# Optimization experiments

Measured on AMD Instinct MI355X. Metric: run time of the kernel, lower is better.

Reference implementation:

```python
import jax, jax.numpy as jnp
import numpy as np

F8_MAX = 448.0  # float8_e4m3fn max
F4_MAX = 6.0    # fp4 e2m1 max
BLOCK = 16      # NVFP4 scaling block size along K

# representable |values| of fp4 e2m1 and midpoints for nearest rounding
_LEVELS = jnp.array([0.0, 0.5, 1.0, 1.5, 2.0, 3.0, 4.0, 6.0], dtype=jnp.float32)
_MIDS = (_LEVELS[:-1] + _LEVELS[1:]) * 0.5


def _e2m1_round(a):
    # round-to-nearest fp4 e2m1 value, sign-magnitude
    s = jnp.sign(a)
    m = jnp.clip(jnp.abs(a), 0.0, F4_MAX)
    idx = jnp.searchsorted(_MIDS, m, side='left')
    return s * jnp.take(_LEVELS, idx)


def _e4m3(x):
    # quantize to float8 e4m3 and dequantize back to fp32
    return jnp.clip(x, -F8_MAX, F8_MAX).astype(jnp.float8_e4m3fn).astype(jnp.float32)


def nvfp4_fake_quant(x, s2):
    # x: [..., K]; s2: scalar global scale = 448*6/global_amax
    shp = x.shape
    K = shp[-1]
    xb = x.reshape(shp[:-1] + (K // BLOCK, BLOCK))  # [..., K/16, 16]
    amax = jnp.max(jnp.abs(xb), axis=-1, keepdims=True)
    sf = _e4m3(amax * s2 / F4_MAX)          # stored per-block fp8 scale (cutlass_vec)
    scale = sf / s2                          # per-block dequant scale in real units
    safe = jnp.where(scale > 0.0, scale, 1.0)
    q = _e2m1_round(xb / safe)               # fp4 codes (as values)
    deq = jnp.where(scale > 0.0, q * scale, 0.0)
    return deq.reshape(shp)


def setup_inputs() -> dict:
    key = jax.random.key(0)
    kx, kw, kb, ks = jax.random.split(key, 4)
    K, N = 4096, 4096
    x = jax.random.normal(kx, (4, 2048, K), dtype=jnp.float32)
    weight = jax.random.uniform(kw, (N, K), dtype=jnp.float32)
    bias = jax.random.uniform(kb, (N,), dtype=jnp.float32)
    # fp4_global_scale of a rand(1, K) tensor, as done in the module __init__
    dummy = jax.random.uniform(ks, (1, K), dtype=jnp.float32)
    s_in2 = ((F8_MAX * F4_MAX) / jnp.max(jnp.abs(dummy))).reshape(1)
    return {'x': x, 'weight': weight, 'bias': bias, 's_in2': s_in2}


def reference(x, weight, bias, s_in2):
    s2_in = s_in2.reshape(())
    s2_w = (F8_MAX * F4_MAX) / jnp.max(jnp.abs(weight))  # fp4_global_scale(weight)
    x_dq = nvfp4_fake_quant(x, s2_in)        # fake-quant activations
    w_dq = nvfp4_fake_quant(weight, s2_w)    # dequantized fp4 weight (stored at init)
    # F.linear: [b,s,k] @ [n,k]^T + bias
    return jnp.einsum('bsk,nk->bsn', x_dq, w_dq) + bias
```

## Files before the change

### kernel.cpp

```cpp
#include <hip/hip_runtime.h>
#include <hip/hip_bf16.h>

typedef __attribute__((ext_vector_type(8))) short short8;
typedef __attribute__((ext_vector_type(8))) unsigned short ushort8;
typedef __attribute__((ext_vector_type(4))) float f32x4;
typedef unsigned short ushort;

#define K_DIM 4096
#define N_DIM 4096
#define BK 32
#define NT (K_DIM / BK)


__device__ __forceinline__ float e4m3_rne(float v) {
    if (v >= 0.015625f) {
        unsigned u = __float_as_uint(v);
        unsigned lsb = (u >> 20) & 1u;
        u = (u + 0x7FFFFu + lsb) & 0xFFF00000u;
        return __uint_as_float(u);
    }
    return rintf(v * 512.0f) * 0.001953125f;
}

__device__ __forceinline__ float e2m1_level(float m) {
    float lv = 0.0f;
    lv = (m > 0.25f) ? 0.5f : lv;
    lv = (m > 0.75f) ? 1.0f : lv;
    lv = (m > 1.25f) ? 1.5f : lv;
    lv = (m > 1.75f) ? 2.0f : lv;
    lv = (m > 2.5f)  ? 3.0f : lv;
    lv = (m > 3.5f)  ? 4.0f : lv;
    lv = (m > 5.0f)  ? 6.0f : lv;
    return lv;
}

__device__ __forceinline__ ushort f32_to_bf16_bits(float f) {
    unsigned u = __float_as_uint(f);
    return (ushort)((u + 0x7FFFu + ((u >> 16) & 1u)) >> 16);
}


__global__ void init_kernel(unsigned* amax_bits) { *amax_bits = 0u; }

__global__ void wamax_kernel(const float* __restrict__ w, unsigned* amax_bits, int n4) {
    float m = 0.f;
    const f32x4* w4 = (const f32x4*)w;
    for (int i = blockIdx.x * blockDim.x + threadIdx.x; i < n4; i += gridDim.x * blockDim.x) {
        f32x4 v = w4[i];
        m = fmaxf(m, fmaxf(fmaxf(fabsf(v.x), fabsf(v.y)), fmaxf(fabsf(v.z), fabsf(v.w))));
    }
#pragma unroll
    for (int off = 32; off >= 1; off >>= 1)
        m = fmaxf(m, __shfl_down(m, off));
    __shared__ float red[4];
    const int lane = threadIdx.x & 63, wv = threadIdx.x >> 6;
    if (lane == 0) red[wv] = m;
    __syncthreads();
    if (threadIdx.x == 0) {
        m = fmaxf(fmaxf(red[0], red[1]), fmaxf(red[2], red[3]));
        atomicMax(amax_bits, __float_as_uint(m));
    }
}

__global__ void quant16_kernel(const float* __restrict__ src,
                               const float* __restrict__ s2_ptr,
                               const unsigned* __restrict__ amax_bits,
                               ushort* __restrict__ dst, int nblk) {
    int t = blockIdx.x * blockDim.x + threadIdx.x;
    if (t >= nblk) return;
    float s2;
    if (s2_ptr) s2 = *s2_ptr;
    else        s2 = 2688.0f / __uint_as_float(*amax_bits);

    const f32x4* s = (const f32x4*)src + (size_t)t * 4;
    float vals[16];
    f32x4 v0 = s[0], v1 = s[1], v2 = s[2], v3 = s[3];
#pragma unroll
    for (int i = 0; i < 4; ++i) {
        vals[i] = v0[i]; vals[4 + i] = v1[i]; vals[8 + i] = v2[i]; vals[12 + i] = v3[i];
    }
    float amax = 0.f;
#pragma unroll
    for (int i = 0; i < 16; ++i) amax = fmaxf(amax, fabsf(vals[i]));

    float sf = e4m3_rne(fminf(amax * s2 / 6.0f, 448.0f));
    float scale = sf / s2;

    ushort8 o0, o1;
    if (scale > 0.f) {
#pragma unroll
        for (int i = 0; i < 16; ++i) {
            float r = vals[i] / scale;
            float m = fminf(fabsf(r), 6.0f);
            float q = copysignf(e2m1_level(m), r);
            ushort b = f32_to_bf16_bits(q * scale);
            if (i < 8) o0[i] = b; else o1[i - 8] = b;
        }
    } else {
#pragma unroll
        for (int i = 0; i < 8; ++i) { o0[i] = 0; o1[i] = 0; }
    }
    ushort8* d8 = (ushort8*)(dst + (size_t)t * 16);
    d8[0] = o0;
    d8[1] = o1;
}


__device__ __forceinline__ void gload16(const ushort* g, ushort* l) {
    __builtin_amdgcn_global_load_lds(
        (const __attribute__((address_space(1))) void*)g,
        (__attribute__((address_space(3))) void*)l, 16, 0, 0);
}

#define SYNC(N)                                              \
    asm volatile("s_waitcnt vmcnt(" #N ")" ::: "memory");    \
    __builtin_amdgcn_sched_barrier(0);                       \
    __builtin_amdgcn_s_barrier();                            \
    __builtin_amdgcn_sched_barrier(0)

__global__ __launch_bounds__(512, 2) void gemm8(
    const ushort* __restrict__ Aq, const ushort* __restrict__ Bq,
    const float* __restrict__ bias, float* __restrict__ C,
    int nby, int nchunk) {
    __shared__ ushort lds[4 * 16384];

    const int tid  = threadIdx.x;
    const int lane = tid & 63;
    const int wave = tid >> 6;
    const int wr = wave >> 2;
    const int wc = wave & 3;

    const int swz = (blockIdx.x & 7) * nchunk + (blockIdx.x >> 3);
    const int by = swz % nby, bx = swz / nby;
    const int bm = by * 256, bn = bx * 256;

    const int r0  = tid >> 2;
    const int cg0 = ((tid & 3) - ((r0 >> 1) & 3)) & 3;
    const ushort* sA0 = Aq + (size_t)(bm + r0) * K_DIM + cg0 * 8;
    const ushort* sB0 = Bq + (size_t)(bn + r0) * K_DIM + cg0 * 8;
    ushort* dA0 = &lds[wave * 512];
    ushort* dB0 = &lds[8192 + wave * 512];

    const int pr   = ((lane >> 4) + ((lane & 15) >> 1)) & 3;
    const int idxA = (wr * 128 + (lane & 15)) * 32 + pr * 8;
    const int idxB = 8192 + (wc * 64 + (lane & 15)) * 32 + pr * 8;

    f32x4 acc[8][4];
#pragma unroll
    for (int m = 0; m < 8; ++m)
#pragma unroll
        for (int n = 0; n < 4; ++n) acc[m][n] = (f32x4)(0.f);

#define STAGE(t) {                                                         \
        const size_t ko = (size_t)(t) * BK;                                \
        const int bb = ((t) & 3) * 16384;                                  \
        gload16(sA0 + ko,                          dA0 + bb);              \
        gload16(sA0 + (size_t)128 * K_DIM + ko,    dA0 + bb + 4096);       \
        gload16(sB0 + ko,                          dB0 + bb);              \
        gload16(sB0 + (size_t)128 * K_DIM + ko,    dB0 + bb + 4096); }

    auto compute = [&](int bufo) {
        const ushort* Lb = &lds[bufo];
        short8 af[8], bfr[4];
#pragma unroll
        for (int m = 0; m < 8; ++m) af[m]  = *(const short8*)(Lb + idxA + m * 512);
#pragma unroll
        for (int n = 0; n < 4; ++n) bfr[n] = *(const short8*)(Lb + idxB + n * 512);
#pragma unroll
        for (int m = 0; m < 8; ++m)
#pragma unroll
            for (int n = 0; n < 4; ++n)
                acc[m][n] = __builtin_amdgcn_mfma_f32_16x16x32_bf16(af[m], bfr[n], acc[m][n], 0, 0, 0);
    };

    STAGE(0); STAGE(1); STAGE(2);
    SYNC(8);

    for (int t = 0; t < NT - 3; ++t) {
        STAGE(t + 3);
        compute((t & 3) * 16384);
        SYNC(8);
    }
    compute(((NT - 3) & 3) * 16384);
    SYNC(4);
    compute(((NT - 2) & 3) * 16384);
    SYNC(0);
    compute(((NT - 1) & 3) * 16384);

    const int fq = lane >> 4, fr = lane & 15;
    float bv[4];
#pragma unroll
    for (int n = 0; n < 4; ++n) bv[n] = bias[bn + wc * 64 + n * 16 + fr];
#pragma unroll
    for (int m = 0; m < 8; ++m)
#pragma unroll
        for (int r = 0; r < 4; ++r) {
            const int row = bm + wr * 128 + m * 16 + fq * 4 + r;
            float* Cr = C + (size_t)row * N_DIM + bn + wc * 64 + fr;
#pragma unroll
            for (int n = 0; n < 4; ++n) Cr[n * 16] = acc[m][n][r] + bv[n];
        }
#undef STAGE
}


extern "C" void kernel_launch(void* const* d_in, const int* in_sizes, int n_in,
                              void* d_out, int out_size, void* d_ws, size_t ws_size,
                              hipStream_t stream) {
    const float* x     = (const float*)d_in[0];
    const float* w     = (const float*)d_in[1];
    const float* bias  = (const float*)d_in[2];
    const float* s_in2 = (const float*)d_in[3];
    float* out = (float*)d_out;

    const int M = in_sizes[0] / K_DIM;

    unsigned* amax_bits = (unsigned*)d_ws;
    ushort* xq = (ushort*)((char*)d_ws + 256);
    ushort* wq = (ushort*)((char*)d_ws + 256 + (size_t)M * K_DIM * 2);

    init_kernel<<<1, 1, 0, stream>>>(amax_bits);
    wamax_kernel<<<1024, 256, 0, stream>>>(w, amax_bits, (N_DIM * K_DIM) / 4);

    const int nblk_x = (M * K_DIM) / 16;
    quant16_kernel<<<nblk_x / 256, 256, 0, stream>>>(x, s_in2, nullptr, xq, nblk_x);
    const int nblk_w = (N_DIM * K_DIM) / 16;
    quant16_kernel<<<nblk_w / 256, 256, 0, stream>>>(w, nullptr, amax_bits, wq, nblk_w);

    const int nby = M / 256;
    const int nwg = nby * (N_DIM / 256);
    gemm8<<<nwg, 512, 0, stream>>>(xq, wq, bias, out, nby, nwg / 8);
}
```

Before: 320.7 us.

## Split GEMM main loop into two barrier-separated phases with interleaved loads and priority

Restructures the GEMM K-loop so each tile is processed in two halves: the first half loads A/B fragments from LDS, issues the A global-to-LDS prefetch, then runs MFMAs at raised wave priority, and the second half does the same with the B prefetch. The aim is to spread global loads and LDS reads across the MFMA work and keep waves in lockstep with extra barriers, ping-pong style. It also replaces the single-thread init kernel with hipMemsetAsync. The extra barriers per iteration add synchronisation cost and may not help if the schedule was already overlapping well.

```diff
diff --git a/kernel.cpp b/kernel.cpp
--- a/kernel.cpp
+++ b/kernel.cpp
@@ -40,8 +40,6 @@
 }
 
 
-__global__ void init_kernel(unsigned* amax_bits) { *amax_bits = 0u; }
-
 __global__ void wamax_kernel(const float* __restrict__ w, unsigned* amax_bits, int n4) {
     float m = 0.f;
     const f32x4* w4 = (const f32x4*)w;
@@ -112,11 +110,7 @@
         (__attribute__((address_space(3))) void*)l, 16, 0, 0);
 }
 
-#define SYNC(N)                                              \
-    asm volatile("s_waitcnt vmcnt(" #N ")" ::: "memory");    \
-    __builtin_amdgcn_sched_barrier(0);                       \
-    __builtin_amdgcn_s_barrier();                            \
-    __builtin_amdgcn_sched_barrier(0)
+#define NOPSTMT ((void)0)
 
 __global__ __launch_bounds__(512, 2) void gemm8(
     const ushort* __restrict__ Aq, const ushort* __restrict__ Bq,
@@ -151,41 +145,90 @@
 #pragma unroll
         for (int n = 0; n < 4; ++n) acc[m][n] = (f32x4)(0.f);
 
-#define STAGE(t) {                                                         \
-        const size_t ko = (size_t)(t) * BK;                                \
-        const int bb = ((t) & 3) * 16384;                                  \
-        gload16(sA0 + ko,                          dA0 + bb);              \
-        gload16(sA0 + (size_t)128 * K_DIM + ko,    dA0 + bb + 4096);       \
-        gload16(sB0 + ko,                          dB0 + bb);              \
-        gload16(sB0 + (size_t)128 * K_DIM + ko,    dB0 + bb + 4096); }
-
-    auto compute = [&](int bufo) {
-        const ushort* Lb = &lds[bufo];
-        short8 af[8], bfr[4];
-#pragma unroll
-        for (int m = 0; m < 8; ++m) af[m]  = *(const short8*)(Lb + idxA + m * 512);
-#pragma unroll
-        for (int n = 0; n < 4; ++n) bfr[n] = *(const short8*)(Lb + idxB + n * 512);
-#pragma unroll
-        for (int m = 0; m < 8; ++m)
-#pragma unroll
-            for (int n = 0; n < 4; ++n)
-                acc[m][n] = __builtin_amdgcn_mfma_f32_16x16x32_bf16(af[m], bfr[n], acc[m][n], 0, 0, 0);
-    };
-
-    STAGE(0); STAGE(1); STAGE(2);
-    SYNC(8);
+    short8 af[8], bfr[4];
+
+#define STAGE_A(t) { const size_t ko = (size_t)(t) * BK;                    \
+        const int bb = ((t) & 3) * 16384;                                   \
+        gload16(sA0 + ko,                       dA0 + bb);                  \
+        gload16(sA0 + (size_t)128 * K_DIM + ko, dA0 + bb + 4096); }
+#define STAGE_B(t) { const size_t ko = (size_t)(t) * BK;                    \
+        const int bb = ((t) & 3) * 16384;                                   \
+        gload16(sB0 + ko,                       dB0 + bb);                  \
+        gload16(sB0 + (size_t)128 * K_DIM + ko, dB0 + bb + 4096); }
+
+#define PHASE0(STAGE_STMT, bufo)                                            \
+    {                                                                       \
+        const ushort* Lb = &lds[bufo];                                      \
+        _Pragma("unroll")                                                   \
+        for (int m = 0; m < 4; ++m) af[m]  = *(const short8*)(Lb + idxA + m * 512); \
+        _Pragma("unroll")                                                   \
+        for (int n = 0; n < 4; ++n) bfr[n] = *(const short8*)(Lb + idxB + n * 512); \
+        STAGE_STMT;                                                         \
+        __builtin_amdgcn_sched_barrier(0);                                  \
+        __builtin_amdgcn_s_barrier();                                       \
+        asm volatile("s_waitcnt lgkmcnt(0)" ::: "memory");                  \
+        __builtin_amdgcn_sched_barrier(0);                                  \
+        __builtin_amdgcn_s_setprio(1);                                      \
+        _Pragma("unroll")                                                   \
+        for (int m = 0; m < 4; ++m)                                         \
+            _Pragma("unroll")                                               \
+            for (int n = 0; n < 4; ++n)                                     \
+                acc[m][n] = __builtin_amdgcn_mfma_f32_16x16x32_bf16(af[m], bfr[n], acc[m][n], 0, 0, 0); \
+        __builtin_amdgcn_s_setprio(0);                                      \
+        __builtin_amdgcn_sched_barrier(0);                                  \
+        __builtin_amdgcn_s_barrier();                                       \
+    }
+
+#define PHASE1(STAGE_STMT, bufo, VN)                                        \
+    {                                                                       \
+        const ushort* Lb = &lds[bufo];                                      \
+        _Pragma("unroll")                                                   \
+        for (int m = 4; m < 8; ++m) af[m] = *(const short8*)(Lb + idxA + m * 512); \
+        STAGE_STMT;                                                         \
+        __builtin_amdgcn_sched_barrier(0);                                  \
+        __builtin_amdgcn_s_barrier();                                       \
+        asm volatile("s_waitcnt lgkmcnt(0)" ::: "memory");                  \
+        __builtin_amdgcn_sched_barrier(0);                                  \
+        __builtin_amdgcn_s_setprio(1);                                      \
+        _Pragma("unroll")                                                   \
+        for (int m = 4; m < 8; ++m)                                         \
+            _Pragma("unroll")                                               \
+            for (int n = 0; n < 4; ++n)                                     \
+                acc[m][n] = __builtin_amdgcn_mfma_f32_16x16x32_bf16(af[m], bfr[n], acc[m][n], 0, 0, 0); \
+        __builtin_amdgcn_s_setprio(0);                                      \
+        __builtin_amdgcn_sched_barrier(0);                                  \
+        asm volatile("s_waitcnt vmcnt(" #VN ")" ::: "memory");              \
+        __builtin_amdgcn_sched_barrier(0);                                  \
+        __builtin_amdgcn_s_barrier();                                       \
+    }
+
+    STAGE_A(0); STAGE_B(0);
+    STAGE_A(1); STAGE_B(1);
+    STAGE_A(2); STAGE_B(2);
+    asm volatile("s_waitcnt vmcnt(8)" ::: "memory");
+    __builtin_amdgcn_sched_barrier(0);
+    __builtin_amdgcn_s_barrier();
 
     for (int t = 0; t < NT - 3; ++t) {
-        STAGE(t + 3);
-        compute((t & 3) * 16384);
-        SYNC(8);
-    }
-    compute(((NT - 3) & 3) * 16384);
-    SYNC(4);
-    compute(((NT - 2) & 3) * 16384);
-    SYNC(0);
-    compute(((NT - 1) & 3) * 16384);
+        const int bufo = (t & 3) * 16384;
+        PHASE0(STAGE_A(t + 3), bufo);
+        PHASE1(STAGE_B(t + 3), bufo, 8);
+    }
+    {
+        const int bufo = ((NT - 3) & 3) * 16384;
+        PHASE0(NOPSTMT, bufo);
+        PHASE1(NOPSTMT, bufo, 4);
+    }
+    {
+        const int bufo = ((NT - 2) & 3) * 16384;
+        PHASE0(NOPSTMT, bufo);
+        PHASE1(NOPSTMT, bufo, 0);
+    }
+    {
+        const int bufo = ((NT - 1) & 3) * 16384;
+        PHASE0(NOPSTMT, bufo);
+        PHASE1(NOPSTMT, bufo, 0);
+    }
 
     const int fq = lane >> 4, fr = lane & 15;
     float bv[4];
@@ -200,7 +243,10 @@
 #pragma unroll
             for (int n = 0; n < 4; ++n) Cr[n * 16] = acc[m][n][r] + bv[n];
         }
-#undef STAGE
+#undef STAGE_A
+#undef STAGE_B
+#undef PHASE0
+#undef PHASE1
 }
 
 
@@ -219,7 +265,7 @@
     ushort* xq = (ushort*)((char*)d_ws + 256);
     ushort* wq = (ushort*)((char*)d_ws + 256 + (size_t)M * K_DIM * 2);
 
-    init_kernel<<<1, 1, 0, stream>>>(amax_bits);
+    hipMemsetAsync(amax_bits, 0, 4, stream);
     wamax_kernel<<<1024, 256, 0, stream>>>(w, amax_bits, (N_DIM * K_DIM) / 4);
 
     const int nblk_x = (M * K_DIM) / 16;
```

After: 327.9 us. +2.2%, slower.
